# Optimization experiments

Hardware: AMD Instinct MI355X
Metric: run time of the kernel (lower is better)

The kernel has to match this reference:

```python
import jax, jax.numpy as jnp
import numpy as np

NUM_LEVELS = 4
N = 524288


def _e8_roots() -> np.ndarray:
    """The 240 roots of the E8 lattice, float32 [240, 8].

    Type 1 (112): all permutations of (+-1, +-1, 0^6).
    Type 2 (128): (+-1/2)^8 with an even number of minus signs.
    """
    roots = []
    for i in range(8):
        for j in range(i + 1, 8):
            for si in (1.0, -1.0):
                for sj in (1.0, -1.0):
                    v = np.zeros(8, dtype=np.float64)
                    v[i] = si
                    v[j] = sj
                    roots.append(v)
    for m in range(256):
        signs = np.array([1.0 if ((m >> k) & 1) == 0 else -1.0 for k in range(8)])
        if int((signs < 0).sum()) % 2 == 0:
            roots.append(0.5 * signs)
    out = np.stack(roots).astype(np.float32)
    assert out.shape == (240, 8)
    return out


def setup_inputs() -> dict:
    key = jax.random.key(0)
    x = jax.random.normal(key, (N, 8), dtype=jnp.float32)
    roots = jnp.asarray(_e8_roots())  # [240, 8] fixed codebook (buffer)
    return {"x": x, "roots": roots}


def reference(x, roots):
    # Residual multi-level nearest-neighbor quantization against E8 roots.
    x_flat = x.reshape(-1, 8)                       # [N, 8]
    r2 = jnp.sum(roots * roots, axis=1)[None, :]    # [1, 240]
    qsum = jnp.zeros_like(x_flat)
    residual = x_flat
    indices = []
    for _level in range(NUM_LEVELS):
        res2 = jnp.sum(residual * residual, axis=1, keepdims=True)      # [N, 1]
        # squared euclidean distances, clamped at 0 for numerical safety
        d2 = jnp.clip(res2 + r2 - 2.0 * (residual @ roots.T), 0.0)      # [N, 240]
        idx = jnp.argmin(d2, axis=-1)                                   # [N]
        qsum = qsum + roots[idx]                                        # gather
        residual = x_flat - qsum
        indices.append(idx)
    quantized = qsum.reshape(x.shape)
    # straight-through estimator: value == quantized, grad flows via x
    quantized_ste = quantized + x - jax.lax.stop_gradient(x)
    qerr = jnp.mean(
        (jax.lax.stop_gradient(x) - jax.lax.stop_gradient(quantized)) ** 2
    )
    idx_stack = jnp.stack(indices).reshape((NUM_LEVELS,) + x.shape[:-1])
    return quantized_ste, idx_stack, qerr
```

## Files before the change

kernel.cpp:

```cpp
#include <hip/hip_runtime.h>
#include <math.h>


__global__ __launch_bounds__(256) void e8_quant_kernel(
    const float* __restrict__ x, const float* __restrict__ roots,
    float* __restrict__ out, float* __restrict__ partials, int nrow) {
#pragma clang fp contract(off)
  __shared__ float lroots[240 * 8];
  __shared__ float wred[4];
  for (int t = threadIdx.x; t < 240 * 8; t += 256) lroots[t] = roots[t];
  __syncthreads();

  const int row = blockIdx.x * 256 + threadIdx.x;
  const bool active = row < nrow;
  float e = 0.f;

  if (active) {
    const float4 xa = *(const float4*)(x + (size_t)row * 8);
    const float4 xb = *(const float4*)(x + (size_t)row * 8 + 4);
    float xr[8] = {xa.x, xa.y, xa.z, xa.w, xb.x, xb.y, xb.z, xb.w};
    float qs[8] = {0.f, 0.f, 0.f, 0.f, 0.f, 0.f, 0.f, 0.f};
    float r[8];
#pragma unroll
    for (int k = 0; k < 8; ++k) r[k] = xr[k];

    float* out_idx = out + (size_t)nrow * 8;

#pragma unroll 1
    for (int lvl = 0; lvl < 4; ++lvl) {
      const float q0 = r[0] * r[0], q1 = r[1] * r[1], q2 = r[2] * r[2],
                  q3 = r[3] * r[3], q4 = r[4] * r[4], q5 = r[5] * r[5],
                  q6 = r[6] * r[6], q7 = r[7] * r[7];
      const float res2 = ((q0 + q1) + (q2 + q3)) + ((q4 + q5) + (q6 + q7));
      const float s = res2 + 2.0f;

      const unsigned u0 = __float_as_uint(r[0]), u1 = __float_as_uint(r[1]),
                     u2 = __float_as_uint(r[2]), u3 = __float_as_uint(r[3]),
                     u4 = __float_as_uint(r[4]), u5 = __float_as_uint(r[5]),
                     u6 = __float_as_uint(r[6]), u7 = __float_as_uint(r[7]);
      const float m0v = __uint_as_float(u0 & 0x7fffffffu),
                  m1v = __uint_as_float(u1 & 0x7fffffffu),
                  m2v = __uint_as_float(u2 & 0x7fffffffu),
                  m3v = __uint_as_float(u3 & 0x7fffffffu),
                  m4v = __uint_as_float(u4 & 0x7fffffffu),
                  m5v = __uint_as_float(u5 & 0x7fffffffu),
                  m6v = __uint_as_float(u6 & 0x7fffffffu),
                  m7v = __uint_as_float(u7 & 0x7fffffffu);
      const int sb0 = (int)(u0 >> 31), sb1 = (int)(u1 >> 31),
                sb2 = (int)(u2 >> 31), sb3 = (int)(u3 >> 31),
                sb4 = (int)(u4 >> 31), sb5 = (int)(u5 >> 31),
                sb6 = (int)(u6 >> 31), sb7 = (int)(u7 >> 31);
      const int msk = sb0 | (sb1 << 1) | (sb2 << 2) | (sb3 << 3) |
                      (sb4 << 4) | (sb5 << 5) | (sb6 << 6) | (sb7 << 7);
      const int par = __popc(msk) & 1;
      const float Sabs =
          ((m0v + m1v) + (m2v + m3v)) + ((m4v + m5v) + (m6v + m7v));

      const int K0 = 0 | (sb0 << 3), K1 = 1 | (sb1 << 3), K2 = 2 | (sb2 << 3),
                K3 = 3 | (sb3 << 3), K4 = 4 | (sb4 << 3), K5 = 5 | (sb5 << 3),
                K6 = 6 | (sb6 << 3), K7 = 7 | (sb7 << 3);

      const bool g01 = m1v > m0v;
      const float h01 = fmaxf(m0v, m1v), l01 = fminf(m0v, m1v);
      const int hk01 = g01 ? K1 : K0, lk01 = g01 ? K0 : K1;
      const bool g23 = m3v > m2v;
      const float h23 = fmaxf(m2v, m3v), l23 = fminf(m2v, m3v);
      const int hk23 = g23 ? K3 : K2, lk23 = g23 ? K2 : K3;
      const bool g45 = m5v > m4v;
      const float h45 = fmaxf(m4v, m5v), l45 = fminf(m4v, m5v);
      const int hk45 = g45 ? K5 : K4, lk45 = g45 ? K4 : K5;
      const bool g67 = m7v > m6v;
      const float h67 = fmaxf(m6v, m7v), l67 = fminf(m6v, m7v);
      const int hk67 = g67 ? K7 : K6, lk67 = g67 ? K6 : K7;
      const bool qg0 = h23 > h01;
      const float qh0 = fmaxf(h01, h23);
      const int qhk0 = qg0 ? hk23 : hk01;
      const float sA0 = qg0 ? l23 : l01;
      const int sAk0 = qg0 ? lk23 : lk01;
      const float sB0 = qg0 ? h01 : h23;
      const int sBk0 = qg0 ? hk01 : hk23;
      const float loL0 = qg0 ? l01 : l23;
      const bool qx0 = sB0 > sA0;
      const float qs0v = fmaxf(sA0, sB0);
      const int qsk0 = qx0 ? sBk0 : sAk0;
      const float qt0 = qx0 ? fmaxf(sA0, loL0) : sB0;
      const bool qg1 = h67 > h45;
      const float qh1 = fmaxf(h45, h67);
      const int qhk1 = qg1 ? hk67 : hk45;
      const float sA1 = qg1 ? l67 : l45;
      const int sAk1 = qg1 ? lk67 : lk45;
      const float sB1 = qg1 ? h45 : h67;
      const int sBk1 = qg1 ? hk45 : hk67;
      const float loL1 = qg1 ? l45 : l67;
      const bool qx1 = sB1 > sA1;
      const float qs1v = fmaxf(sA1, sB1);
      const int qsk1 = qx1 ? sBk1 : sAk1;
      const float qt1 = qx1 ? fmaxf(sA1, loL1) : sB1;
      const bool fg = qh1 > qh0;
      const float A1v = fmaxf(qh0, qh1);
      const int A1K = fg ? qhk1 : qhk0;
      const float fA = fg ? qs1v : qs0v;
      const int fAk = fg ? qsk1 : qsk0;
      const float fB = fg ? qh0 : qh1;
      const int fBk = fg ? qhk0 : qhk1;
      const float tW = fg ? qt1 : qt0;
      const float sL = fg ? qs0v : qs1v;
      const bool fh = fB > fA;
      const float A2v = fmaxf(fA, fB);
      const int A2K = fh ? fBk : fAk;
      const float A3v = fh ? fmaxf(fA, sL) : fmaxf(tW, fB);

      const bool n0 = l23 < l01;
      const float mn0 = fminf(l01, l23);
      const int mnk0 = n0 ? lk23 : lk01;
      const float pr0 = n0 ? h23 : h01;
      const float ot0 = fmaxf(l01, l23);
      const bool n1 = l67 < l45;
      const float mn1 = fminf(l45, l67);
      const int mnk1 = n1 ? lk67 : lk45;
      const float pr1 = n1 ? h67 : h45;
      const float ot1 = fmaxf(l45, l67);
      const bool nf = mn1 < mn0;
      const float Aminv = fminf(mn0, mn1);
      const int AminK = nf ? mnk1 : mnk0;
      const float prW = nf ? pr1 : pr0;
      const float otW = nf ? ot1 : ot0;
      const float mnL = fmaxf(mn0, mn1);
      const float Amin2v = fminf(prW, fminf(otW, mnL));

      const float dT1r = A1v + A2v;
      const float halfS = 0.5f * Sabs;
      const float dT2 = par ? (halfS - Aminv) : halfS;

      const int p1 = A1K & 7, p2 = A2K & 7;
      const int s1b = A1K >> 3, s2b = A2K >> 3;
      const bool o12 = p1 < p2;
      const int imn = o12 ? p1 : p2, jmx = o12 ? p2 : p1;
      const int sIb = o12 ? s1b : s2b, sJb = o12 ? s2b : s1b;
      const int pbase = imn * 7 - ((imn * (imn - 1)) >> 1) + (jmx - imn - 1);
      const int t1idx = (pbase << 2) | (sIb << 1) | sJb;

      const int mp = AminK & 7;
      const int mf = par ? (msk ^ (1 << mp)) : msk;
      const int t2idx = 112 + (mf >> 1);

      const float thr =
          (res2 + 2.0f * Sabs + 2.0f) * 1.9073486e-06f;
      const bool a1 = (A2v - A3v) > thr;
      const bool a2 = par ? ((Amin2v - Aminv) > thr)
                          : ((Aminv + Amin2v) > thr);
      const bool c = fabsf(dT1r - dT2) > thr;

      float d1 = fmaf(-2.f, dT1r, s);
      int i1 = t1idx;
      float d2x = 0.f;
      int i2 = t2idx;

      if (__any(!a1)) {
        if (!a1) {
          float best = 3.4028235e38f;
          int be = 0;
          int ci = 0;
#pragma unroll
          for (int i = 0; i < 8; ++i) {
#pragma unroll
            for (int j = i + 1; j < 8; ++j) {
              const float a = r[i] + r[j];
              const float b = r[i] - r[j];
              float d;
              d = fmaf(-2.f, a, s);
              if (d < best) { best = d; be = ci + 0; }
              d = fmaf(-2.f, b, s);
              if (d < best) { best = d; be = ci + 1; }
              d = fmaf(2.f, b, s);
              if (d < best) { best = d; be = ci + 2; }
              d = fmaf(2.f, a, s);
              if (d < best) { best = d; be = ci + 3; }
              ci += 4;
            }
          }
          d1 = best;
          i1 = be;
        }
      }

      if (__any(!a2)) {
        if (!a2) {
          const float h0 = 0.5f * r[0], h1 = 0.5f * r[1], h2 = 0.5f * r[2],
                      h3 = 0.5f * r[3], h4 = 0.5f * r[4], h5 = 0.5f * r[5],
                      h6 = 0.5f * r[6], h7 = 0.5f * r[7];
          float best2 = 3.4028235e38f;
          int bt = 0;
#pragma unroll
          for (int t = 0; t < 128; ++t) {
            const int m = (t << 1) | (__popc(t) & 1);
            float v = (m & 1) ? -h0 : h0;
            v = (m & 2) ? (v - h1) : (v + h1);
            v = (m & 4) ? (v - h2) : (v + h2);
            v = (m & 8) ? (v - h3) : (v + h3);
            v = (m & 16) ? (v - h4) : (v + h4);
            v = (m & 32) ? (v - h5) : (v + h5);
            v = (m & 64) ? (v - h6) : (v + h6);
            v = (m & 128) ? (v - h7) : (v + h7);
            const float d = fmaf(-2.f, v, s);
            if (d < best2) { best2 = d; bt = t; }
          }
          d2x = best2;
          i2 = 112 + bt;
        }
      }

      if (__any(!c && a2)) {
        if (!c && a2) {
          const int flip = par ? mp : 8;
          float t0 = 0.5f * m0v, t1v = 0.5f * m1v, t2v = 0.5f * m2v,
                t3v = 0.5f * m3v, t4v = 0.5f * m4v, t5v = 0.5f * m5v,
                t6v = 0.5f * m6v, t7v = 0.5f * m7v;
          t0 = (flip == 0) ? -t0 : t0;
          t1v = (flip == 1) ? -t1v : t1v;
          t2v = (flip == 2) ? -t2v : t2v;
          t3v = (flip == 3) ? -t3v : t3v;
          t4v = (flip == 4) ? -t4v : t4v;
          t5v = (flip == 5) ? -t5v : t5v;
          t6v = (flip == 6) ? -t6v : t6v;
          t7v = (flip == 7) ? -t7v : t7v;
          float v = t0;
          v = v + t1v;
          v = v + t2v;
          v = v + t3v;
          v = v + t4v;
          v = v + t5v;
          v = v + t6v;
          v = v + t7v;
          d2x = fmaf(-2.f, v, s);
        }
      }

      const int bi = c ? ((dT1r > dT2) ? i1 : i2)
                       : ((d1 <= d2x) ? i1 : i2);

      out_idx[(size_t)lvl * nrow + row] = (float)bi;

      const float4 ra = *(const float4*)(lroots + bi * 8);
      const float4 rb = *(const float4*)(lroots + bi * 8 + 4);
      qs[0] += ra.x; qs[1] += ra.y; qs[2] += ra.z; qs[3] += ra.w;
      qs[4] += rb.x; qs[5] += rb.y; qs[6] += rb.z; qs[7] += rb.w;
#pragma unroll
      for (int k = 0; k < 8; ++k) r[k] = xr[k] - qs[k];
    }

    float o[8];
#pragma unroll
    for (int k = 0; k < 8; ++k) o[k] = (qs[k] + xr[k]) - xr[k];
    *(float4*)(out + (size_t)row * 8) = make_float4(o[0], o[1], o[2], o[3]);
    *(float4*)(out + (size_t)row * 8 + 4) = make_float4(o[4], o[5], o[6], o[7]);

#pragma unroll
    for (int k = 0; k < 8; ++k) e = fmaf(r[k], r[k], e);
  }

#pragma unroll
  for (int off = 32; off > 0; off >>= 1) e += __shfl_down(e, off, 64);
  const int lane = threadIdx.x & 63, wv = threadIdx.x >> 6;
  if (lane == 0) wred[wv] = e;
  __syncthreads();
  if (threadIdx.x == 0)
    partials[blockIdx.x] = (wred[0] + wred[1]) + (wred[2] + wred[3]);
}

__global__ __launch_bounds__(256) void qerr_reduce_kernel(
    const float* __restrict__ partials, float* __restrict__ out, int n,
    size_t pos, float scale) {
#pragma clang fp contract(off)
  __shared__ float wred[4];
  float e = 0.f;
  for (int i = threadIdx.x; i < n; i += 256) e += partials[i];
#pragma unroll
  for (int off = 32; off > 0; off >>= 1) e += __shfl_down(e, off, 64);
  const int lane = threadIdx.x & 63, wv = threadIdx.x >> 6;
  if (lane == 0) wred[wv] = e;
  __syncthreads();
  if (threadIdx.x == 0)
    out[pos] = ((wred[0] + wred[1]) + (wred[2] + wred[3])) * scale;
}

extern "C" void kernel_launch(void* const* d_in, const int* in_sizes, int n_in,
                              void* d_out, int out_size, void* d_ws,
                              size_t ws_size, hipStream_t stream) {
  const float* x = (const float*)d_in[0];
  const float* roots = (const float*)d_in[1];
  float* out = (float*)d_out;
  float* partials = (float*)d_ws;

  const int nrow = in_sizes[0] / 8;
  const int nblocks = (nrow + 255) / 256;

  e8_quant_kernel<<<nblocks, 256, 0, stream>>>(x, roots, out, partials, nrow);

  const size_t qerr_pos = (size_t)nrow * 12;
  const float scale = 1.0f / (float)((size_t)nrow * 8);
  qerr_reduce_kernel<<<1, 256, 0, stream>>>(partials, out, nblocks, qerr_pos,
                                            scale);
}
```

Measured before the change: 92.89 us.

## Process two rows per thread and add cheap fallback paths for ambiguous cases

Each thread now handles two rows, so the grid is half as large and the shared root table is loaded once per 512 rows instead of per 256. The ambiguous type-1 fallback gets a 28-candidate sign-aligned search when the smallest magnitude clears the threshold, and the type-2 fallback gets an 8-candidate single-flip search instead of scanning all 128. The tie threshold is tightened from about 2^-19 to 2^-20 relative. This targets the divergent full-scan cost. It raises register pressure, and the narrower threshold could change tie-breaking agreement with the reference.

```diff
diff --git a/kernel.cpp b/kernel.cpp
--- a/kernel.cpp
+++ b/kernel.cpp
@@ -7,157 +7,181 @@
     float* __restrict__ out, float* __restrict__ partials, int nrow) {
 #pragma clang fp contract(off)
   __shared__ float lroots[240 * 8];
-  __shared__ float wred[4];
+  __shared__ float wred0[4];
+  __shared__ float wred1[4];
   for (int t = threadIdx.x; t < 240 * 8; t += 256) lroots[t] = roots[t];
   __syncthreads();
 
-  const int row = blockIdx.x * 256 + threadIdx.x;
-  const bool active = row < nrow;
-  float e = 0.f;
-
-  if (active) {
-    const float4 xa = *(const float4*)(x + (size_t)row * 8);
-    const float4 xb = *(const float4*)(x + (size_t)row * 8 + 4);
-    float xr[8] = {xa.x, xa.y, xa.z, xa.w, xb.x, xb.y, xb.z, xb.w};
-    float qs[8] = {0.f, 0.f, 0.f, 0.f, 0.f, 0.f, 0.f, 0.f};
-    float r[8];
-#pragma unroll
-    for (int k = 0; k < 8; ++k) r[k] = xr[k];
-
-    float* out_idx = out + (size_t)nrow * 8;
-
-#pragma unroll 1
-    for (int lvl = 0; lvl < 4; ++lvl) {
-      const float q0 = r[0] * r[0], q1 = r[1] * r[1], q2 = r[2] * r[2],
-                  q3 = r[3] * r[3], q4 = r[4] * r[4], q5 = r[5] * r[5],
-                  q6 = r[6] * r[6], q7 = r[7] * r[7];
-      const float res2 = ((q0 + q1) + (q2 + q3)) + ((q4 + q5) + (q6 + q7));
-      const float s = res2 + 2.0f;
-
-      const unsigned u0 = __float_as_uint(r[0]), u1 = __float_as_uint(r[1]),
-                     u2 = __float_as_uint(r[2]), u3 = __float_as_uint(r[3]),
-                     u4 = __float_as_uint(r[4]), u5 = __float_as_uint(r[5]),
-                     u6 = __float_as_uint(r[6]), u7 = __float_as_uint(r[7]);
-      const float m0v = __uint_as_float(u0 & 0x7fffffffu),
-                  m1v = __uint_as_float(u1 & 0x7fffffffu),
-                  m2v = __uint_as_float(u2 & 0x7fffffffu),
-                  m3v = __uint_as_float(u3 & 0x7fffffffu),
-                  m4v = __uint_as_float(u4 & 0x7fffffffu),
-                  m5v = __uint_as_float(u5 & 0x7fffffffu),
-                  m6v = __uint_as_float(u6 & 0x7fffffffu),
-                  m7v = __uint_as_float(u7 & 0x7fffffffu);
-      const int sb0 = (int)(u0 >> 31), sb1 = (int)(u1 >> 31),
-                sb2 = (int)(u2 >> 31), sb3 = (int)(u3 >> 31),
-                sb4 = (int)(u4 >> 31), sb5 = (int)(u5 >> 31),
-                sb6 = (int)(u6 >> 31), sb7 = (int)(u7 >> 31);
-      const int msk = sb0 | (sb1 << 1) | (sb2 << 2) | (sb3 << 3) |
-                      (sb4 << 4) | (sb5 << 5) | (sb6 << 6) | (sb7 << 7);
-      const int par = __popc(msk) & 1;
-      const float Sabs =
-          ((m0v + m1v) + (m2v + m3v)) + ((m4v + m5v) + (m6v + m7v));
-
-      const int K0 = 0 | (sb0 << 3), K1 = 1 | (sb1 << 3), K2 = 2 | (sb2 << 3),
-                K3 = 3 | (sb3 << 3), K4 = 4 | (sb4 << 3), K5 = 5 | (sb5 << 3),
-                K6 = 6 | (sb6 << 3), K7 = 7 | (sb7 << 3);
-
-      const bool g01 = m1v > m0v;
-      const float h01 = fmaxf(m0v, m1v), l01 = fminf(m0v, m1v);
-      const int hk01 = g01 ? K1 : K0, lk01 = g01 ? K0 : K1;
-      const bool g23 = m3v > m2v;
-      const float h23 = fmaxf(m2v, m3v), l23 = fminf(m2v, m3v);
-      const int hk23 = g23 ? K3 : K2, lk23 = g23 ? K2 : K3;
-      const bool g45 = m5v > m4v;
-      const float h45 = fmaxf(m4v, m5v), l45 = fminf(m4v, m5v);
-      const int hk45 = g45 ? K5 : K4, lk45 = g45 ? K4 : K5;
-      const bool g67 = m7v > m6v;
-      const float h67 = fmaxf(m6v, m7v), l67 = fminf(m6v, m7v);
-      const int hk67 = g67 ? K7 : K6, lk67 = g67 ? K6 : K7;
-      const bool qg0 = h23 > h01;
-      const float qh0 = fmaxf(h01, h23);
-      const int qhk0 = qg0 ? hk23 : hk01;
-      const float sA0 = qg0 ? l23 : l01;
-      const int sAk0 = qg0 ? lk23 : lk01;
-      const float sB0 = qg0 ? h01 : h23;
-      const int sBk0 = qg0 ? hk01 : hk23;
-      const float loL0 = qg0 ? l01 : l23;
-      const bool qx0 = sB0 > sA0;
-      const float qs0v = fmaxf(sA0, sB0);
-      const int qsk0 = qx0 ? sBk0 : sAk0;
-      const float qt0 = qx0 ? fmaxf(sA0, loL0) : sB0;
-      const bool qg1 = h67 > h45;
-      const float qh1 = fmaxf(h45, h67);
-      const int qhk1 = qg1 ? hk67 : hk45;
-      const float sA1 = qg1 ? l67 : l45;
-      const int sAk1 = qg1 ? lk67 : lk45;
-      const float sB1 = qg1 ? h45 : h67;
-      const int sBk1 = qg1 ? hk45 : hk67;
-      const float loL1 = qg1 ? l45 : l67;
-      const bool qx1 = sB1 > sA1;
-      const float qs1v = fmaxf(sA1, sB1);
-      const int qsk1 = qx1 ? sBk1 : sAk1;
-      const float qt1 = qx1 ? fmaxf(sA1, loL1) : sB1;
-      const bool fg = qh1 > qh0;
-      const float A1v = fmaxf(qh0, qh1);
-      const int A1K = fg ? qhk1 : qhk0;
-      const float fA = fg ? qs1v : qs0v;
-      const int fAk = fg ? qsk1 : qsk0;
-      const float fB = fg ? qh0 : qh1;
-      const int fBk = fg ? qhk0 : qhk1;
-      const float tW = fg ? qt1 : qt0;
-      const float sL = fg ? qs0v : qs1v;
-      const bool fh = fB > fA;
-      const float A2v = fmaxf(fA, fB);
-      const int A2K = fh ? fBk : fAk;
-      const float A3v = fh ? fmaxf(fA, sL) : fmaxf(tW, fB);
-
-      const bool n0 = l23 < l01;
-      const float mn0 = fminf(l01, l23);
-      const int mnk0 = n0 ? lk23 : lk01;
-      const float pr0 = n0 ? h23 : h01;
-      const float ot0 = fmaxf(l01, l23);
-      const bool n1 = l67 < l45;
-      const float mn1 = fminf(l45, l67);
-      const int mnk1 = n1 ? lk67 : lk45;
-      const float pr1 = n1 ? h67 : h45;
-      const float ot1 = fmaxf(l45, l67);
-      const bool nf = mn1 < mn0;
-      const float Aminv = fminf(mn0, mn1);
-      const int AminK = nf ? mnk1 : mnk0;
-      const float prW = nf ? pr1 : pr0;
-      const float otW = nf ? ot1 : ot0;
-      const float mnL = fmaxf(mn0, mn1);
-      const float Amin2v = fminf(prW, fminf(otW, mnL));
-
-      const float dT1r = A1v + A2v;
-      const float halfS = 0.5f * Sabs;
-      const float dT2 = par ? (halfS - Aminv) : halfS;
-
-      const int p1 = A1K & 7, p2 = A2K & 7;
-      const int s1b = A1K >> 3, s2b = A2K >> 3;
-      const bool o12 = p1 < p2;
-      const int imn = o12 ? p1 : p2, jmx = o12 ? p2 : p1;
-      const int sIb = o12 ? s1b : s2b, sJb = o12 ? s2b : s1b;
-      const int pbase = imn * 7 - ((imn * (imn - 1)) >> 1) + (jmx - imn - 1);
-      const int t1idx = (pbase << 2) | (sIb << 1) | sJb;
-
-      const int mp = AminK & 7;
-      const int mf = par ? (msk ^ (1 << mp)) : msk;
-      const int t2idx = 112 + (mf >> 1);
-
-      const float thr =
-          (res2 + 2.0f * Sabs + 2.0f) * 1.9073486e-06f;
-      const bool a1 = (A2v - A3v) > thr;
-      const bool a2 = par ? ((Amin2v - Aminv) > thr)
-                          : ((Aminv + Amin2v) > thr);
-      const bool c = fabsf(dT1r - dT2) > thr;
-
-      float d1 = fmaf(-2.f, dT1r, s);
-      int i1 = t1idx;
-      float d2x = 0.f;
-      int i2 = t2idx;
-
-      if (__any(!a1)) {
-        if (!a1) {
+  const int row0 = blockIdx.x * 512 + threadIdx.x;
+  const int row1 = row0 + 256;
+  const bool act0 = row0 < nrow;
+  const bool act1 = row1 < nrow;
+  float* out_idx = out + (size_t)nrow * 8;
+
+  float xr0[8], qs0[8], r0[8];
+  float xr1[8], qs1[8], r1[8];
+  float e0 = 0.f, e1 = 0.f;
+
+  if (act0) {
+    const float4 xa = *(const float4*)(x + (size_t)row0 * 8);
+    const float4 xb = *(const float4*)(x + (size_t)row0 * 8 + 4);
+    xr0[0] = xa.x; xr0[1] = xa.y; xr0[2] = xa.z; xr0[3] = xa.w;
+    xr0[4] = xb.x; xr0[5] = xb.y; xr0[6] = xb.z; xr0[7] = xb.w;
+#pragma unroll
+    for (int k = 0; k < 8; ++k) { qs0[k] = 0.f; r0[k] = xr0[k]; }
+  }
+  if (act1) {
+    const float4 xa = *(const float4*)(x + (size_t)row1 * 8);
+    const float4 xb = *(const float4*)(x + (size_t)row1 * 8 + 4);
+    xr1[0] = xa.x; xr1[1] = xa.y; xr1[2] = xa.z; xr1[3] = xa.w;
+    xr1[4] = xb.x; xr1[5] = xb.y; xr1[6] = xb.z; xr1[7] = xb.w;
+#pragma unroll
+    for (int k = 0; k < 8; ++k) { qs1[k] = 0.f; r1[k] = xr1[k]; }
+  }
+
+  auto level_step = [&](int lvl, float (&xr)[8], float (&qs)[8],
+                        float (&r)[8], int row) {
+    float q[8];
+#pragma unroll
+    for (int k = 0; k < 8; ++k) q[k] = r[k] * r[k];
+    const float res2 = ((q[0] + q[1]) + (q[2] + q[3])) +
+                       ((q[4] + q[5]) + (q[6] + q[7]));
+    const float s = res2 + 2.0f;
+
+    float mg[8];
+    int sb[8];
+#pragma unroll
+    for (int k = 0; k < 8; ++k) {
+      const unsigned u = __float_as_uint(r[k]);
+      mg[k] = __uint_as_float(u & 0x7fffffffu);
+      sb[k] = (int)(u >> 31);
+    }
+    const int msk = sb[0] | (sb[1] << 1) | (sb[2] << 2) | (sb[3] << 3) |
+                    (sb[4] << 4) | (sb[5] << 5) | (sb[6] << 6) | (sb[7] << 7);
+    const int par = __popc(msk) & 1;
+    const float Sabs = ((mg[0] + mg[1]) + (mg[2] + mg[3])) +
+                       ((mg[4] + mg[5]) + (mg[6] + mg[7]));
+
+    const int K0 = 0 | (sb[0] << 3), K1 = 1 | (sb[1] << 3),
+              K2 = 2 | (sb[2] << 3), K3 = 3 | (sb[3] << 3),
+              K4 = 4 | (sb[4] << 3), K5 = 5 | (sb[5] << 3),
+              K6 = 6 | (sb[6] << 3), K7 = 7 | (sb[7] << 3);
+
+    const bool g01 = mg[1] > mg[0];
+    const float h01 = fmaxf(mg[0], mg[1]), l01 = fminf(mg[0], mg[1]);
+    const int hk01 = g01 ? K1 : K0, lk01 = g01 ? K0 : K1;
+    const bool g23 = mg[3] > mg[2];
+    const float h23 = fmaxf(mg[2], mg[3]), l23 = fminf(mg[2], mg[3]);
+    const int hk23 = g23 ? K3 : K2, lk23 = g23 ? K2 : K3;
+    const bool g45 = mg[5] > mg[4];
+    const float h45 = fmaxf(mg[4], mg[5]), l45 = fminf(mg[4], mg[5]);
+    const int hk45 = g45 ? K5 : K4, lk45 = g45 ? K4 : K5;
+    const bool g67 = mg[7] > mg[6];
+    const float h67 = fmaxf(mg[6], mg[7]), l67 = fminf(mg[6], mg[7]);
+    const int hk67 = g67 ? K7 : K6, lk67 = g67 ? K6 : K7;
+    const bool qg0 = h23 > h01;
+    const float qh0 = fmaxf(h01, h23);
+    const int qhk0 = qg0 ? hk23 : hk01;
+    const float sA0 = qg0 ? l23 : l01;
+    const int sAk0 = qg0 ? lk23 : lk01;
+    const float sB0 = qg0 ? h01 : h23;
+    const int sBk0 = qg0 ? hk01 : hk23;
+    const float loL0 = qg0 ? l01 : l23;
+    const bool qx0 = sB0 > sA0;
+    const float qs0v = fmaxf(sA0, sB0);
+    const int qsk0 = qx0 ? sBk0 : sAk0;
+    const float qt0 = qx0 ? fmaxf(sA0, loL0) : sB0;
+    const bool qg1 = h67 > h45;
+    const float qh1 = fmaxf(h45, h67);
+    const int qhk1 = qg1 ? hk67 : hk45;
+    const float sA1 = qg1 ? l67 : l45;
+    const int sAk1 = qg1 ? lk67 : lk45;
+    const float sB1 = qg1 ? h45 : h67;
+    const int sBk1 = qg1 ? hk45 : hk67;
+    const float loL1 = qg1 ? l45 : l67;
+    const bool qx1 = sB1 > sA1;
+    const float qs1v = fmaxf(sA1, sB1);
+    const int qsk1 = qx1 ? sBk1 : sAk1;
+    const float qt1 = qx1 ? fmaxf(sA1, loL1) : sB1;
+    const bool fg = qh1 > qh0;
+    const float A1v = fmaxf(qh0, qh1);
+    const int A1K = fg ? qhk1 : qhk0;
+    const float fA = fg ? qs1v : qs0v;
+    const int fAk = fg ? qsk1 : qsk0;
+    const float fB = fg ? qh0 : qh1;
+    const int fBk = fg ? qhk0 : qhk1;
+    const float tW = fg ? qt1 : qt0;
+    const float sL = fg ? qs0v : qs1v;
+    const bool fh = fB > fA;
+    const float A2v = fmaxf(fA, fB);
+    const int A2K = fh ? fBk : fAk;
+    const float A3v = fh ? fmaxf(fA, sL) : fmaxf(tW, fB);
+
+    const bool n0 = l23 < l01;
+    const float mn0 = fminf(l01, l23);
+    const int mnk0 = n0 ? lk23 : lk01;
+    const float pr0 = n0 ? h23 : h01;
+    const float ot0 = fmaxf(l01, l23);
+    const bool n1 = l67 < l45;
+    const float mn1 = fminf(l45, l67);
+    const int mnk1 = n1 ? lk67 : lk45;
+    const float pr1 = n1 ? h67 : h45;
+    const float ot1 = fmaxf(l45, l67);
+    const bool nf = mn1 < mn0;
+    const float Aminv = fminf(mn0, mn1);
+    const int AminK = nf ? mnk1 : mnk0;
+    const float prW = nf ? pr1 : pr0;
+    const float otW = nf ? ot1 : ot0;
+    const float mnL = fmaxf(mn0, mn1);
+    const float Amin2v = fminf(prW, fminf(otW, mnL));
+
+    const float dT1r = A1v + A2v;
+    const float halfS = 0.5f * Sabs;
+    const float dT2 = par ? (halfS - Aminv) : halfS;
+
+    const int p1 = A1K & 7, p2 = A2K & 7;
+    const int s1b = A1K >> 3, s2b = A2K >> 3;
+    const bool o12 = p1 < p2;
+    const int imn = o12 ? p1 : p2, jmx = o12 ? p2 : p1;
+    const int sIb = o12 ? s1b : s2b, sJb = o12 ? s2b : s1b;
+    const int pbase = imn * 7 - ((imn * (imn - 1)) >> 1) + (jmx - imn - 1);
+    const int t1idx = (pbase << 2) | (sIb << 1) | sJb;
+
+    const int mp = AminK & 7;
+    const int mf = par ? (msk ^ (1 << mp)) : msk;
+    const int t2idx = 112 + (mf >> 1);
+
+    const float thr = (res2 + 2.0f * Sabs + 2.0f) * 0x1.0p-20f;
+    const bool a1 = (A2v - A3v) > thr;
+    const bool a2 = par ? ((Amin2v - Aminv) > thr)
+                        : ((Aminv + Amin2v) > thr);
+    const bool c = fabsf(dT1r - dT2) > thr;
+
+    float d1 = fmaf(-2.f, dT1r, s);
+    int i1 = t1idx;
+    float d2x = 0.f;
+    int i2 = t2idx;
+
+    if (__any(!a1)) {
+      if (!a1) {
+        if (Aminv > thr) {
+          float best = 3.4028235e38f;
+          int bidx = 0;
+          int ci = 0;
+#pragma unroll
+          for (int i = 0; i < 8; ++i) {
+#pragma unroll
+            for (int j = i + 1; j < 8; ++j) {
+              const float aa = mg[i] + mg[j];
+              const float d = fmaf(-2.f, aa, s);
+              const int idx = (ci << 2) | (sb[i] << 1) | sb[j];
+              if (d < best) { best = d; bidx = idx; }
+              ++ci;
+            }
+          }
+          d1 = best;
+          i1 = bidx;
+        } else {
           float best = 3.4028235e38f;
           int be = 0;
           int ci = 0;
@@ -183,25 +207,42 @@
           i1 = be;
         }
       }
-
-      if (__any(!a2)) {
-        if (!a2) {
-          const float h0 = 0.5f * r[0], h1 = 0.5f * r[1], h2 = 0.5f * r[2],
-                      h3 = 0.5f * r[3], h4 = 0.5f * r[4], h5 = 0.5f * r[5],
-                      h6 = 0.5f * r[6], h7 = 0.5f * r[7];
+    }
+
+    if (__any(!a2)) {
+      if (!a2) {
+        float h[8];
+#pragma unroll
+        for (int k = 0; k < 8; ++k) h[k] = 0.5f * r[k];
+        const bool cheap = par && ((Amin2v + Amin2v) > thr);
+        if (cheap) {
           float best2 = 3.4028235e38f;
           int bt = 0;
 #pragma unroll
+          for (int k = 0; k < 8; ++k) {
+            const int mk = msk ^ (1 << k);
+            float v = (mk & 1) ? -h[0] : h[0];
+#pragma unroll
+            for (int j = 1; j < 8; ++j)
+              v = (mk & (1 << j)) ? (v - h[j]) : (v + h[j]);
+            const float d = fmaf(-2.f, v, s);
+            const int t = mk >> 1;
+            const bool take = (d < best2) || (d == best2 && t < bt);
+            best2 = take ? d : best2;
+            bt = take ? t : bt;
+          }
+          d2x = best2;
+          i2 = 112 + bt;
+        } else {
+          float best2 = 3.4028235e38f;
+          int bt = 0;
+#pragma unroll 1
           for (int t = 0; t < 128; ++t) {
             const int m = (t << 1) | (__popc(t) & 1);
-            float v = (m & 1) ? -h0 : h0;
-            v = (m & 2) ? (v - h1) : (v + h1);
-            v = (m & 4) ? (v - h2) : (v + h2);
-            v = (m & 8) ? (v - h3) : (v + h3);
-            v = (m & 16) ? (v - h4) : (v + h4);
-            v = (m & 32) ? (v - h5) : (v + h5);
-            v = (m & 64) ? (v - h6) : (v + h6);
-            v = (m & 128) ? (v - h7) : (v + h7);
+            float v = (m & 1) ? -h[0] : h[0];
+#pragma unroll
+            for (int j = 1; j < 8; ++j)
+              v = (m & (1 << j)) ? (v - h[j]) : (v + h[j]);
             const float d = fmaf(-2.f, v, s);
             if (d < best2) { best2 = d; bt = t; }
           }
@@ -209,63 +250,74 @@
           i2 = 112 + bt;
         }
       }
-
-      if (__any(!c && a2)) {
-        if (!c && a2) {
-          const int flip = par ? mp : 8;
-          float t0 = 0.5f * m0v, t1v = 0.5f * m1v, t2v = 0.5f * m2v,
-                t3v = 0.5f * m3v, t4v = 0.5f * m4v, t5v = 0.5f * m5v,
-                t6v = 0.5f * m6v, t7v = 0.5f * m7v;
-          t0 = (flip == 0) ? -t0 : t0;
-          t1v = (flip == 1) ? -t1v : t1v;
-          t2v = (flip == 2) ? -t2v : t2v;
-          t3v = (flip == 3) ? -t3v : t3v;
-          t4v = (flip == 4) ? -t4v : t4v;
-          t5v = (flip == 5) ? -t5v : t5v;
-          t6v = (flip == 6) ? -t6v : t6v;
-          t7v = (flip == 7) ? -t7v : t7v;
-          float v = t0;
-          v = v + t1v;
-          v = v + t2v;
-          v = v + t3v;
-          v = v + t4v;
-          v = v + t5v;
-          v = v + t6v;
-          v = v + t7v;
-          d2x = fmaf(-2.f, v, s);
+    }
+
+    if (__any(!c && a2)) {
+      if (!c && a2) {
+        const int flip = par ? mp : 8;
+        float v = (flip == 0) ? -(0.5f * mg[0]) : (0.5f * mg[0]);
+#pragma unroll
+        for (int j = 1; j < 8; ++j) {
+          const float tj = 0.5f * mg[j];
+          v = (flip == j) ? (v - tj) : (v + tj);
         }
+        d2x = fmaf(-2.f, v, s);
       }
-
-      const int bi = c ? ((dT1r > dT2) ? i1 : i2)
-                       : ((d1 <= d2x) ? i1 : i2);
-
-      out_idx[(size_t)lvl * nrow + row] = (float)bi;
-
-      const float4 ra = *(const float4*)(lroots + bi * 8);
-      const float4 rb = *(const float4*)(lroots + bi * 8 + 4);
-      qs[0] += ra.x; qs[1] += ra.y; qs[2] += ra.z; qs[3] += ra.w;
-      qs[4] += rb.x; qs[5] += rb.y; qs[6] += rb.z; qs[7] += rb.w;
-#pragma unroll
-      for (int k = 0; k < 8; ++k) r[k] = xr[k] - qs[k];
     }
 
+    const int bi = c ? ((dT1r > dT2) ? i1 : i2)
+                     : ((d1 <= d2x) ? i1 : i2);
+
+    out_idx[(size_t)lvl * nrow + row] = (float)bi;
+
+    const float4 ra = *(const float4*)(lroots + bi * 8);
+    const float4 rb = *(const float4*)(lroots + bi * 8 + 4);
+    qs[0] += ra.x; qs[1] += ra.y; qs[2] += ra.z; qs[3] += ra.w;
+    qs[4] += rb.x; qs[5] += rb.y; qs[6] += rb.z; qs[7] += rb.w;
+#pragma unroll
+    for (int k = 0; k < 8; ++k) r[k] = xr[k] - qs[k];
+  };
+
+#pragma unroll 1
+  for (int lvl = 0; lvl < 4; ++lvl) {
+    if (act0) level_step(lvl, xr0, qs0, r0, row0);
+    if (act1) level_step(lvl, xr1, qs1, r1, row1);
+  }
+
+  if (act0) {
     float o[8];
 #pragma unroll
-    for (int k = 0; k < 8; ++k) o[k] = (qs[k] + xr[k]) - xr[k];
-    *(float4*)(out + (size_t)row * 8) = make_float4(o[0], o[1], o[2], o[3]);
-    *(float4*)(out + (size_t)row * 8 + 4) = make_float4(o[4], o[5], o[6], o[7]);
-
-#pragma unroll
-    for (int k = 0; k < 8; ++k) e = fmaf(r[k], r[k], e);
-  }
-
-#pragma unroll
-  for (int off = 32; off > 0; off >>= 1) e += __shfl_down(e, off, 64);
+    for (int k = 0; k < 8; ++k) o[k] = (qs0[k] + xr0[k]) - xr0[k];
+    *(float4*)(out + (size_t)row0 * 8) = make_float4(o[0], o[1], o[2], o[3]);
+    *(float4*)(out + (size_t)row0 * 8 + 4) =
+        make_float4(o[4], o[5], o[6], o[7]);
+#pragma unroll
+    for (int k = 0; k < 8; ++k) e0 = fmaf(r0[k], r0[k], e0);
+  }
+  if (act1) {
+    float o[8];
+#pragma unroll
+    for (int k = 0; k < 8; ++k) o[k] = (qs1[k] + xr1[k]) - xr1[k];
+    *(float4*)(out + (size_t)row1 * 8) = make_float4(o[0], o[1], o[2], o[3]);
+    *(float4*)(out + (size_t)row1 * 8 + 4) =
+        make_float4(o[4], o[5], o[6], o[7]);
+#pragma unroll
+    for (int k = 0; k < 8; ++k) e1 = fmaf(r1[k], r1[k], e1);
+  }
+
+#pragma unroll
+  for (int off = 32; off > 0; off >>= 1) e0 += __shfl_down(e0, off, 64);
+#pragma unroll
+  for (int off = 32; off > 0; off >>= 1) e1 += __shfl_down(e1, off, 64);
   const int lane = threadIdx.x & 63, wv = threadIdx.x >> 6;
-  if (lane == 0) wred[wv] = e;
+  if (lane == 0) { wred0[wv] = e0; wred1[wv] = e1; }
   __syncthreads();
-  if (threadIdx.x == 0)
-    partials[blockIdx.x] = (wred[0] + wred[1]) + (wred[2] + wred[3]);
+  if (threadIdx.x == 0) {
+    partials[2 * blockIdx.x] =
+        (wred0[0] + wred0[1]) + (wred0[2] + wred0[3]);
+    partials[2 * blockIdx.x + 1] =
+        (wred1[0] + wred1[1]) + (wred1[2] + wred1[3]);
+  }
 }
 
 __global__ __launch_bounds__(256) void qerr_reduce_kernel(
@@ -293,12 +345,12 @@
   float* partials = (float*)d_ws;
 
   const int nrow = in_sizes[0] / 8;
-  const int nblocks = (nrow + 255) / 256;
+  const int nblocks = (nrow + 511) / 512;
 
   e8_quant_kernel<<<nblocks, 256, 0, stream>>>(x, roots, out, partials, nrow);
 
   const size_t qerr_pos = (size_t)nrow * 12;
   const float scale = 1.0f / (float)((size_t)nrow * 8);
-  qerr_reduce_kernel<<<1, 256, 0, stream>>>(partials, out, nblocks, qerr_pos,
-                                            scale);
+  qerr_reduce_kernel<<<1, 256, 0, stream>>>(partials, out, 2 * nblocks,
+                                            qerr_pos, scale);
 }
```

After: 90.28 us. -2.8%, faster.
